# Kernel optimization log

Hardware: AMD Instinct MI355X
Metric: run time of the kernel (lower is better)

Reference implementation:

```python
import jax, jax.numpy as jnp
import numpy as np
import math

N_QUBITS = 8
N_LAYERS = 2
EMBED = 512
HEADS = 64
B, T = 2, 1024


def _ry(state, theta, wire, off):
    # state: (batch?, 2, 2, ..., 2); theta: scalar or (N,)
    ax = off + wire
    st = jnp.moveaxis(state, ax, -1)
    s0, s1 = st[..., 0], st[..., 1]
    half = jnp.asarray(theta) * 0.5
    c, s = jnp.cos(half), jnp.sin(half)
    if c.ndim:  # batched angles -> broadcast over remaining qubit axes
        c = c.reshape((-1,) + (1,) * (s0.ndim - 1))
        s = s.reshape((-1,) + (1,) * (s0.ndim - 1))
    new = jnp.stack([c * s0 - s * s1, s * s0 + c * s1], axis=-1)
    return jnp.moveaxis(new, -1, ax)


def _cnot(state, cw, tw, off):
    st = jnp.moveaxis(state, (off + cw, off + tw), (-2, -1))
    new = jnp.stack([st[..., 0, :], st[..., 1, ::-1]], axis=-2)
    return jnp.moveaxis(new, (-2, -1), (off + cw, off + tw))


def _entangling_state(params):
    # Fixed-parameter block applied to |0...0>: single shared statevector.
    n = N_QUBITS
    psi = jnp.zeros((2,) * n, dtype=params.dtype).at[(0,) * n].set(1.0)
    for l in range(N_LAYERS):
        for q in range(n):
            psi = _ry(psi, params[l, q], q, 0)
        for q in range(n - 1):
            psi = _cnot(psi, q, q + 1, 0)
        psi = _cnot(psi, n - 1, 0, 0)
    return psi


def _quantum_heads(angles, params):
    # angles: (N, n_qubits) data-encoding RY angles; returns (N, n_qubits) <Z_q>.
    n = N_QUBITS
    psi0 = _entangling_state(params)
    state = jnp.broadcast_to(psi0, (angles.shape[0],) + (2,) * n)
    for q in range(n):
        state = _ry(state, angles[:, q], q, 1)
    probs = state * state  # real statevector -> probabilities
    zs = []
    for q in range(n):
        axes = tuple(a for a in range(1, n + 1) if a != q + 1)
        m = probs.sum(axes)  # (N, 2)
        zs.append(m[:, 0] - m[:, 1])
    return jnp.stack(zs, axis=-1)


def setup_inputs() -> dict:
    key = jax.random.key(0)
    kx, kq, kk, kv, kp = jax.random.split(key, 5)
    scale = 1.0 / math.sqrt(EMBED)
    return {
        "x": jax.random.normal(kx, (B, T, EMBED), dtype=jnp.float32),
        "Wq": jax.random.normal(kq, (EMBED, EMBED), dtype=jnp.float32) * scale,
        "Wk": jax.random.normal(kk, (EMBED, EMBED), dtype=jnp.float32) * scale,
        "Wv": jax.random.normal(kv, (EMBED, EMBED), dtype=jnp.float32) * scale,
        "params": jax.random.normal(kp, (N_LAYERS, N_QUBITS), dtype=jnp.float32),
    }


def reference(x, Wq, Wk, Wv, params):
    Bx, Tx, E = x.shape
    head_dim = E // HEADS
    q = x @ Wq.T
    k = x @ Wk.T
    v = x @ Wv.T
    # NOTE: attention on the full embed dim (no head split), scaled by sqrt(E).
    scores = jnp.einsum("bte,bse->bts", q, k) / jnp.sqrt(jnp.asarray(E, x.dtype))
    weights = jax.nn.softmax(scores, axis=-1)
    out = jnp.einsum("bts,bse->bte", weights, v)
    heads = out.reshape(Bx, Tx, HEADS, head_dim)[..., :N_QUBITS]
    angles = heads.reshape(-1, N_QUBITS)  # (B*T*HEADS, n_qubits)
    z = _quantum_heads(angles, params)
    return z.reshape(Bx, Tx, HEADS * N_QUBITS)
```

## Files before the change

kernel.cpp:

```cpp
#include <hip/hip_runtime.h>
#include <math.h>

typedef __attribute__((ext_vector_type(8))) short bf16x8;
typedef __attribute__((ext_vector_type(4))) float f32x4;

#define LD 72

__device__ __forceinline__ ushort f2b(float f) {
    unsigned u = __float_as_uint(f);
    return (ushort)((u + 0x7FFFu + ((u >> 16) & 1u)) >> 16);
}

__global__ __launch_bounds__(256) void cvt_kernel(const float* __restrict__ x,
                                                  const float* __restrict__ wq,
                                                  const float* __restrict__ wk,
                                                  const float* __restrict__ wv,
                                                  ushort* __restrict__ xb,
                                                  ushort* __restrict__ wqb,
                                                  ushort* __restrict__ wkb,
                                                  ushort* __restrict__ wvb) {
    const int z = blockIdx.y;
    const float* src = (z == 0) ? x : (z == 1) ? wq : (z == 2) ? wk : wv;
    ushort* dst = (z == 0) ? xb : (z == 1) ? wqb : (z == 2) ? wkb : wvb;
    const int n = (z == 0) ? (2048 * 512) : (512 * 512);
    const int i = (blockIdx.x * 256 + threadIdx.x) * 8;
    if (i >= n) return;
    float4 v0 = *(const float4*)(src + i);
    float4 v1 = *(const float4*)(src + i + 4);
    ushort t[8] = {f2b(v0.x), f2b(v0.y), f2b(v0.z), f2b(v0.w),
                   f2b(v1.x), f2b(v1.y), f2b(v1.z), f2b(v1.w)};
    *(uint4*)(dst + i) = *(uint4*)t;
}

__global__ __launch_bounds__(256) void qconsts_kernel(const float* __restrict__ params,
                                                      float* __restrict__ ab) {
    __shared__ float st[256];
    __shared__ float red[64];
    const int tid = threadIdx.x;
    st[tid] = (tid == 0) ? 1.0f : 0.0f;
    __syncthreads();
    for (int l = 0; l < 2; ++l) {
        for (int q = 0; q < 8; ++q) {
            float h = 0.5f * params[l * 8 + q];
            float c = cosf(h), s = sinf(h);
            int str = 1 << (7 - q);
            if ((tid & str) == 0) {
                float s0 = st[tid], s1 = st[tid + str];
                st[tid]       = c * s0 - s * s1;
                st[tid + str] = s * s0 + c * s1;
            }
            __syncthreads();
        }
        for (int q = 0; q < 8; ++q) {
            int cw = q, tw = (q + 1) & 7;
            int cs = 1 << (7 - cw), ts = 1 << (7 - tw);
            if ((tid & cs) && !(tid & ts)) {
                float a = st[tid], b = st[tid ^ ts];
                st[tid] = b;
                st[tid ^ ts] = a;
            }
            __syncthreads();
        }
    }
    const float amp = st[tid];
    float v[16];
#pragma unroll
    for (int q = 0; q < 8; ++q) {
        int str = 1 << (7 - q);
        v[q]     = amp * amp * ((tid & str) ? -1.0f : 1.0f);
        v[8 + q] = ((tid & str) == 0) ? 2.0f * amp * st[tid ^ str] : 0.0f;
    }
#pragma unroll
    for (int off = 32; off; off >>= 1)
#pragma unroll
        for (int q = 0; q < 16; ++q) v[q] += __shfl_xor(v[q], off);
    const int lane = tid & 63, wid = tid >> 6;
    if (lane == 0)
#pragma unroll
        for (int q = 0; q < 16; ++q) red[wid * 16 + q] = v[q];
    __syncthreads();
    if (tid < 16) ab[tid] = red[tid] + red[16 + tid] + red[32 + tid] + red[48 + tid];
}

__device__ __forceinline__ void load64(const ushort* __restrict__ p, int ld, int k0,
                                       int tid, uint4 r[2]) {
#pragma unroll
    for (int c = 0; c < 2; ++c) {
        int idx = tid + 256 * c;
        int row = idx >> 3, col = (idx & 7) * 8;
        r[c] = *(const uint4*)(p + (size_t)row * ld + k0 + col);
    }
}
__device__ __forceinline__ void store64(short (*S)[LD], int tid, const uint4 r[2]) {
#pragma unroll
    for (int c = 0; c < 2; ++c) {
        int idx = tid + 256 * c;
        int row = idx >> 3, col = (idx & 7) * 8;
        *(uint4*)&S[row][col] = r[c];
    }
}

__device__ __forceinline__ void mfma64(const short (*As)[LD], const short (*Bs)[LD],
                                       f32x4 acc[2][2], int lane, int wr, int wc) {
    const int r = lane & 15, kb = (lane >> 4) * 8;
#pragma unroll
    for (int c = 0; c < 2; ++c) {
        const int k = c * 32 + kb;
        bf16x8 a0 = *(const bf16x8*)&As[wr * 32 + r][k];
        bf16x8 a1 = *(const bf16x8*)&As[wr * 32 + 16 + r][k];
        bf16x8 b0 = *(const bf16x8*)&Bs[wc * 32 + r][k];
        bf16x8 b1 = *(const bf16x8*)&Bs[wc * 32 + 16 + r][k];
        acc[0][0] = __builtin_amdgcn_mfma_f32_16x16x32_bf16(a0, b0, acc[0][0], 0, 0, 0);
        acc[0][1] = __builtin_amdgcn_mfma_f32_16x16x32_bf16(a0, b1, acc[0][1], 0, 0, 0);
        acc[1][0] = __builtin_amdgcn_mfma_f32_16x16x32_bf16(a1, b0, acc[1][0], 0, 0, 0);
        acc[1][1] = __builtin_amdgcn_mfma_f32_16x16x32_bf16(a1, b1, acc[1][1], 0, 0, 0);
    }
}

__global__ __launch_bounds__(256) void qkv_mfma(const ushort* __restrict__ xb,
                                                const ushort* __restrict__ wqb,
                                                const ushort* __restrict__ wkb,
                                                const ushort* __restrict__ wvb,
                                                ushort* __restrict__ qb,
                                                ushort* __restrict__ kb,
                                                ushort* __restrict__ vT) {
    __shared__ short As[2][64][LD];
    __shared__ short Bs[2][64][LD];
    const int tid = threadIdx.x, lane = tid & 63, w = tid >> 6;
    const int wr = w >> 1, wc = w & 1;
    const int z = blockIdx.z;
    int m0, n0, ldc;
    const ushort *A, *B;
    ushort* C;
    if (z < 2) {
        m0 = blockIdx.x << 6;  n0 = blockIdx.y << 6;
        A = xb;  B = (z == 0) ? wqb : wkb;  C = (z == 0) ? qb : kb;  ldc = 512;
    } else {
        m0 = blockIdx.y << 6;  n0 = blockIdx.x << 6;
        A = wvb;  B = xb;  C = vT;  ldc = 2048;
    }
    const ushort* Ap = A + (size_t)m0 * 512;
    const ushort* Bp = B + (size_t)n0 * 512;
    uint4 ra[2], rb[2];
    load64(Ap, 512, 0, tid, ra);
    load64(Bp, 512, 0, tid, rb);
    store64(As[0], tid, ra);
    store64(Bs[0], tid, rb);
    __syncthreads();
    f32x4 acc[2][2] = {};
    for (int t = 0; t < 8; ++t) {
        if (t < 7) {
            load64(Ap, 512, (t + 1) * 64, tid, ra);
            load64(Bp, 512, (t + 1) * 64, tid, rb);
        }
        mfma64(As[t & 1], Bs[t & 1], acc, lane, wr, wc);
        if (t < 7) {
            store64(As[(t & 1) ^ 1], tid, ra);
            store64(Bs[(t & 1) ^ 1], tid, rb);
        }
        __syncthreads();
    }
    const int rb2 = (lane >> 4) << 2, cc = lane & 15;
#pragma unroll
    for (int fr = 0; fr < 2; ++fr)
#pragma unroll
        for (int fc = 0; fc < 2; ++fc) {
            int row = m0 + wr * 32 + fr * 16 + rb2;
            int col = n0 + wc * 32 + fc * 16 + cc;
#pragma unroll
            for (int r = 0; r < 4; ++r)
                C[(size_t)(row + r) * ldc + col] = f2b(acc[fr][fc][r]);
        }
}

__global__ __launch_bounds__(256) void scores_mfma(const ushort* __restrict__ qb,
                                                   const ushort* __restrict__ kb,
                                                   float* __restrict__ sb) {
    __shared__ short As[2][64][LD];
    __shared__ short Bs[2][64][LD];
    const int tid = threadIdx.x, lane = tid & 63, w = tid >> 6;
    const int wr = w >> 1, wc = w & 1;
    const int m0 = blockIdx.x << 6, n0 = blockIdx.y << 6, z = blockIdx.z;
    const ushort* Ap = qb + (size_t)z * 1024 * 512 + (size_t)m0 * 512;
    const ushort* Bp = kb + (size_t)z * 1024 * 512 + (size_t)n0 * 512;
    float* C = sb + (size_t)z * 1024 * 1024;
    uint4 ra[2], rb[2];
    load64(Ap, 512, 0, tid, ra);
    load64(Bp, 512, 0, tid, rb);
    store64(As[0], tid, ra);
    store64(Bs[0], tid, rb);
    __syncthreads();
    f32x4 acc[2][2] = {};
    for (int t = 0; t < 8; ++t) {
        if (t < 7) {
            load64(Ap, 512, (t + 1) * 64, tid, ra);
            load64(Bp, 512, (t + 1) * 64, tid, rb);
        }
        mfma64(As[t & 1], Bs[t & 1], acc, lane, wr, wc);
        if (t < 7) {
            store64(As[(t & 1) ^ 1], tid, ra);
            store64(Bs[(t & 1) ^ 1], tid, rb);
        }
        __syncthreads();
    }
    const float scale = 0.044194173824159216f;
    const int rb2 = (lane >> 4) << 2, cc = lane & 15;
#pragma unroll
    for (int fr = 0; fr < 2; ++fr)
#pragma unroll
        for (int fc = 0; fc < 2; ++fc) {
            int row = m0 + wr * 32 + fr * 16 + rb2;
            int col = n0 + wc * 32 + fc * 16 + cc;
#pragma unroll
            for (int r = 0; r < 4; ++r)
                C[(size_t)(row + r) * 1024 + col] = acc[fr][fc][r] * scale;
        }
}

__global__ __launch_bounds__(256) void softmax_kernel(const float* __restrict__ S,
                                                      ushort* __restrict__ W) {
    const int row = blockIdx.x, tid = threadIdx.x;
    const float* p = S + (size_t)row * 1024;
    float4 v = ((const float4*)p)[tid];
    float m = fmaxf(fmaxf(v.x, v.y), fmaxf(v.z, v.w));
#pragma unroll
    for (int off = 32; off; off >>= 1) m = fmaxf(m, __shfl_xor(m, off));
    __shared__ float sm[4];
    __shared__ float ss[4];
    const int wid = tid >> 6, lane = tid & 63;
    if (lane == 0) sm[wid] = m;
    __syncthreads();
    m = fmaxf(fmaxf(sm[0], sm[1]), fmaxf(sm[2], sm[3]));
    float e0 = expf(v.x - m), e1 = expf(v.y - m), e2 = expf(v.z - m), e3 = expf(v.w - m);
    float s = e0 + e1 + e2 + e3;
#pragma unroll
    for (int off = 32; off; off >>= 1) s += __shfl_xor(s, off);
    if (lane == 0) ss[wid] = s;
    __syncthreads();
    s = ss[0] + ss[1] + ss[2] + ss[3];
    float r = 1.0f / s;
    ushort4 o = {f2b(e0 * r), f2b(e1 * r), f2b(e2 * r), f2b(e3 * r)};
    ((ushort4*)(W + (size_t)row * 1024))[tid] = o;
}

__global__ __launch_bounds__(256) void pv_mfma(const ushort* __restrict__ wb,
                                               const ushort* __restrict__ vT,
                                               float* __restrict__ out,
                                               const float* __restrict__ ab) {
    __shared__ short As[2][32][LD];
    __shared__ short Bs[2][64][LD];
    const int tid = threadIdx.x, lane = tid & 63, w = tid >> 6;
    const int wr = w >> 1, wc = w & 1;
    const int m0 = blockIdx.x << 5, n0 = blockIdx.y << 6, z = blockIdx.z;
    const ushort* Ap = wb + (size_t)z * 1024 * 1024 + (size_t)m0 * 1024;
    const ushort* Bp = vT + (size_t)n0 * 2048 + z * 1024;
    float* C = out + (size_t)z * 1024 * 512;

    uint4 ra, rbv[2];
    const int arow = tid >> 3, acol = (tid & 7) * 8;
    ra = *(const uint4*)(Ap + (size_t)arow * 1024 + acol);
    load64(Bp, 2048, 0, tid, rbv);
    *(uint4*)&As[0][arow][acol] = ra;
    store64(Bs[0], tid, rbv);
    __syncthreads();
    f32x4 acc[2] = {};
    for (int t = 0; t < 16; ++t) {
        if (t < 15) {
            ra = *(const uint4*)(Ap + (size_t)arow * 1024 + (t + 1) * 64 + acol);
            load64(Bp, 2048, (t + 1) * 64, tid, rbv);
        }
        {
            const short (*Asb)[LD] = As[t & 1];
            const short (*Bsb)[LD] = Bs[t & 1];
            const int r = lane & 15, kb = (lane >> 4) * 8;
#pragma unroll
            for (int c = 0; c < 2; ++c) {
                const int k = c * 32 + kb;
                bf16x8 a0 = *(const bf16x8*)&Asb[wr * 16 + r][k];
                bf16x8 b0 = *(const bf16x8*)&Bsb[wc * 32 + r][k];
                bf16x8 b1 = *(const bf16x8*)&Bsb[wc * 32 + 16 + r][k];
                acc[0] = __builtin_amdgcn_mfma_f32_16x16x32_bf16(a0, b0, acc[0], 0, 0, 0);
                acc[1] = __builtin_amdgcn_mfma_f32_16x16x32_bf16(a0, b1, acc[1], 0, 0, 0);
            }
        }
        if (t < 15) {
            *(uint4*)&As[(t & 1) ^ 1][arow][acol] = ra;
            store64(Bs[(t & 1) ^ 1], tid, rbv);
        }
        __syncthreads();
    }
    const float Aq = ab[lane & 7], Bq = ab[8 + (lane & 7)];
    const int rb2 = (lane >> 4) << 2, cc = lane & 15;
#pragma unroll
    for (int fc = 0; fc < 2; ++fc) {
        int row = m0 + wr * 16 + rb2;
        int col = n0 + wc * 32 + fc * 16 + cc;
#pragma unroll
        for (int r = 0; r < 4; ++r) {
            float sn, cs;
            sincosf(acc[fc][r], &sn, &cs);
            C[(size_t)(row + r) * 512 + col] = cs * Aq - sn * Bq;
        }
    }
}

extern "C" void kernel_launch(void* const* d_in, const int* in_sizes, int n_in,
                              void* d_out, int out_size, void* d_ws, size_t ws_size,
                              hipStream_t stream) {
    const float* x      = (const float*)d_in[0];
    const float* Wq     = (const float*)d_in[1];
    const float* Wk     = (const float*)d_in[2];
    const float* Wv     = (const float*)d_in[3];
    const float* params = (const float*)d_in[4];
    float* out = (float*)d_out;

    char* base = (char*)d_ws;
    float*  ab  = (float*)base;
    ushort* xb  = (ushort*)(base + 256);
    ushort* wqb = xb + 2048 * 512;
    ushort* wkb = wqb + 512 * 512;
    ushort* wvb = wkb + 512 * 512;
    ushort* qb  = wvb + 512 * 512;
    ushort* kb  = qb + 2048 * 512;
    ushort* vT  = kb + 2048 * 512;
    float*  sb  = (float*)(vT + 2048 * 512);
    ushort* wb  = (ushort*)(sb + 2 * 1024 * 1024);

    hipLaunchKernelGGL(cvt_kernel, dim3(512, 4), dim3(256), 0, stream,
                       x, Wq, Wk, Wv, xb, wqb, wkb, wvb);
    hipLaunchKernelGGL(qconsts_kernel, dim3(1), dim3(256), 0, stream, params, ab);
    hipLaunchKernelGGL(qkv_mfma, dim3(32, 8, 3), dim3(256), 0, stream,
                       xb, wqb, wkb, wvb, qb, kb, vT);
    hipLaunchKernelGGL(scores_mfma, dim3(16, 16, 2), dim3(256), 0, stream, qb, kb, sb);
    hipLaunchKernelGGL(softmax_kernel, dim3(2048), dim3(256), 0, stream, sb, wb);
    hipLaunchKernelGGL(pv_mfma, dim3(32, 8, 2), dim3(256), 0, stream, wb, vT, out, ab);
}
```

Before: 106.2 us.

## Stage GEMM tiles with direct global-to-LDS loads and XOR swizzle, enlarge tiles

Replaces the register-staged global→LDS copies in all three MFMA GEMMs with global_load_lds direct transfers into an XOR-swizzled unpadded LDS layout. The QKV GEMM moves to 128x128 tiles with 4x4 MFMA fragments per wave, and the PV GEMM to 64x64 tiles. The bf16 conversion and quantum-constant kernels are merged into one launch. This removes VGPR round-trips and one kernel launch, and increases data reuse. The cost is fewer blocks for occupancy and reliance on async LDS load ordering being correct around barriers.

Result: slower. 111.3 us (+4.8%).

```diff
diff --git a/kernel.cpp b/kernel.cpp
--- a/kernel.cpp
+++ b/kernel.cpp
@@ -3,40 +3,108 @@
 
 typedef __attribute__((ext_vector_type(8))) short bf16x8;
 typedef __attribute__((ext_vector_type(4))) float f32x4;
-
-#define LD 72
 
 __device__ __forceinline__ ushort f2b(float f) {
     unsigned u = __float_as_uint(f);
     return (ushort)((u + 0x7FFFu + ((u >> 16) & 1u)) >> 16);
 }
 
-__global__ __launch_bounds__(256) void cvt_kernel(const float* __restrict__ x,
-                                                  const float* __restrict__ wq,
-                                                  const float* __restrict__ wk,
-                                                  const float* __restrict__ wv,
-                                                  ushort* __restrict__ xb,
-                                                  ushort* __restrict__ wqb,
-                                                  ushort* __restrict__ wkb,
-                                                  ushort* __restrict__ wvb) {
-    const int z = blockIdx.y;
-    const float* src = (z == 0) ? x : (z == 1) ? wq : (z == 2) ? wk : wv;
-    ushort* dst = (z == 0) ? xb : (z == 1) ? wqb : (z == 2) ? wkb : wvb;
-    const int n = (z == 0) ? (2048 * 512) : (512 * 512);
-    const int i = (blockIdx.x * 256 + threadIdx.x) * 8;
-    if (i >= n) return;
-    float4 v0 = *(const float4*)(src + i);
-    float4 v1 = *(const float4*)(src + i + 4);
-    ushort t[8] = {f2b(v0.x), f2b(v0.y), f2b(v0.z), f2b(v0.w),
-                   f2b(v1.x), f2b(v1.y), f2b(v1.z), f2b(v1.w)};
-    *(uint4*)(dst + i) = *(uint4*)t;
-}
-
-__global__ __launch_bounds__(256) void qconsts_kernel(const float* __restrict__ params,
-                                                      float* __restrict__ ab) {
+__device__ __forceinline__ void gl16(const ushort* g, ushort* l) {
+    __builtin_amdgcn_global_load_lds((const __attribute__((address_space(1))) void*)g,
+                                     (__attribute__((address_space(3))) void*)l, 16, 0, 0);
+}
+
+__device__ __forceinline__ void stage128(const ushort* g, int ld, ushort* lds,
+                                         int w, int lane) {
+    const int rsub = lane >> 3;
+    const size_t coff = (size_t)(((lane & 7) ^ (rsub & 7)) * 8);
+#pragma unroll
+    for (int ii = 0; ii < 4; ++ii) {
+        const int i = w * 4 + ii;
+        gl16(g + (size_t)(i * 8 + rsub) * ld + coff, lds + i * 512);
+    }
+}
+__device__ __forceinline__ void stage64(const ushort* g, int ld, ushort* lds,
+                                        int w, int lane) {
+    const int rsub = lane >> 3;
+    const size_t coff = (size_t)(((lane & 7) ^ (rsub & 7)) * 8);
+#pragma unroll
+    for (int ii = 0; ii < 2; ++ii) {
+        const int i = w * 2 + ii;
+        gl16(g + (size_t)(i * 8 + rsub) * ld + coff, lds + i * 512);
+    }
+}
+
+__device__ __forceinline__ bf16x8 frag(const ushort* lds, int row0, int c, int lane) {
+    const int r = row0 + (lane & 15);
+    const int slot = (c * 4 + (lane >> 4)) ^ (r & 7);
+    return *(const bf16x8*)(lds + (size_t)r * 64 + slot * 8);
+}
+
+__device__ __forceinline__ void compute128(const ushort* As, const ushort* Bs,
+                                           f32x4 acc[4][4], int lane, int wr, int wc) {
+#pragma unroll
+    for (int c = 0; c < 2; ++c) {
+        bf16x8 a[4], b[4];
+#pragma unroll
+        for (int f = 0; f < 4; ++f) {
+            a[f] = frag(As, wr * 64 + f * 16, c, lane);
+            b[f] = frag(Bs, wc * 64 + f * 16, c, lane);
+        }
+#pragma unroll
+        for (int i = 0; i < 4; ++i)
+#pragma unroll
+            for (int j = 0; j < 4; ++j)
+                acc[i][j] = __builtin_amdgcn_mfma_f32_16x16x32_bf16(a[i], b[j], acc[i][j], 0, 0, 0);
+    }
+}
+
+__device__ __forceinline__ void compute64(const ushort* As, const ushort* Bs,
+                                          f32x4 acc[2][2], int lane, int wr, int wc) {
+#pragma unroll
+    for (int c = 0; c < 2; ++c) {
+        bf16x8 a[2], b[2];
+#pragma unroll
+        for (int f = 0; f < 2; ++f) {
+            a[f] = frag(As, wr * 32 + f * 16, c, lane);
+            b[f] = frag(Bs, wc * 32 + f * 16, c, lane);
+        }
+#pragma unroll
+        for (int i = 0; i < 2; ++i)
+#pragma unroll
+            for (int j = 0; j < 2; ++j)
+                acc[i][j] = __builtin_amdgcn_mfma_f32_16x16x32_bf16(a[i], b[j], acc[i][j], 0, 0, 0);
+    }
+}
+
+__global__ __launch_bounds__(256) void cvtq_kernel(const float* __restrict__ x,
+                                                   const float* __restrict__ wq,
+                                                   const float* __restrict__ wk,
+                                                   const float* __restrict__ wv,
+                                                   const float* __restrict__ params,
+                                                   ushort* __restrict__ xb,
+                                                   ushort* __restrict__ wqb,
+                                                   ushort* __restrict__ wkb,
+                                                   ushort* __restrict__ wvb,
+                                                   float* __restrict__ ab) {
+    const int tid = threadIdx.x;
+    if (blockIdx.y < 4) {
+        const int z = blockIdx.y;
+        const float* src = (z == 0) ? x : (z == 1) ? wq : (z == 2) ? wk : wv;
+        ushort* dst = (z == 0) ? xb : (z == 1) ? wqb : (z == 2) ? wkb : wvb;
+        const int n = (z == 0) ? (2048 * 512) : (512 * 512);
+        const int i = (blockIdx.x * 256 + tid) * 8;
+        if (i >= n) return;
+        float4 v0 = *(const float4*)(src + i);
+        float4 v1 = *(const float4*)(src + i + 4);
+        ushort t[8] = {f2b(v0.x), f2b(v0.y), f2b(v0.z), f2b(v0.w),
+                       f2b(v1.x), f2b(v1.y), f2b(v1.z), f2b(v1.w)};
+        *(uint4*)(dst + i) = *(uint4*)t;
+        return;
+    }
+    if (blockIdx.x != 0) return;
     __shared__ float st[256];
     __shared__ float red[64];
-    const int tid = threadIdx.x;
     st[tid] = (tid == 0) ? 1.0f : 0.0f;
     __syncthreads();
     for (int l = 0; l < 2; ++l) {
@@ -82,41 +150,6 @@
     if (tid < 16) ab[tid] = red[tid] + red[16 + tid] + red[32 + tid] + red[48 + tid];
 }
 
-__device__ __forceinline__ void load64(const ushort* __restrict__ p, int ld, int k0,
-                                       int tid, uint4 r[2]) {
-#pragma unroll
-    for (int c = 0; c < 2; ++c) {
-        int idx = tid + 256 * c;
-        int row = idx >> 3, col = (idx & 7) * 8;
-        r[c] = *(const uint4*)(p + (size_t)row * ld + k0 + col);
-    }
-}
-__device__ __forceinline__ void store64(short (*S)[LD], int tid, const uint4 r[2]) {
-#pragma unroll
-    for (int c = 0; c < 2; ++c) {
-        int idx = tid + 256 * c;
-        int row = idx >> 3, col = (idx & 7) * 8;
-        *(uint4*)&S[row][col] = r[c];
-    }
-}
-
-__device__ __forceinline__ void mfma64(const short (*As)[LD], const short (*Bs)[LD],
-                                       f32x4 acc[2][2], int lane, int wr, int wc) {
-    const int r = lane & 15, kb = (lane >> 4) * 8;
-#pragma unroll
-    for (int c = 0; c < 2; ++c) {
-        const int k = c * 32 + kb;
-        bf16x8 a0 = *(const bf16x8*)&As[wr * 32 + r][k];
-        bf16x8 a1 = *(const bf16x8*)&As[wr * 32 + 16 + r][k];
-        bf16x8 b0 = *(const bf16x8*)&Bs[wc * 32 + r][k];
-        bf16x8 b1 = *(const bf16x8*)&Bs[wc * 32 + 16 + r][k];
-        acc[0][0] = __builtin_amdgcn_mfma_f32_16x16x32_bf16(a0, b0, acc[0][0], 0, 0, 0);
-        acc[0][1] = __builtin_amdgcn_mfma_f32_16x16x32_bf16(a0, b1, acc[0][1], 0, 0, 0);
-        acc[1][0] = __builtin_amdgcn_mfma_f32_16x16x32_bf16(a1, b0, acc[1][0], 0, 0, 0);
-        acc[1][1] = __builtin_amdgcn_mfma_f32_16x16x32_bf16(a1, b1, acc[1][1], 0, 0, 0);
-    }
-}
-
 __global__ __launch_bounds__(256) void qkv_mfma(const ushort* __restrict__ xb,
                                                 const ushort* __restrict__ wqb,
                                                 const ushort* __restrict__ wkb,
@@ -124,8 +157,8 @@
                                                 ushort* __restrict__ qb,
                                                 ushort* __restrict__ kb,
                                                 ushort* __restrict__ vT) {
-    __shared__ short As[2][64][LD];
-    __shared__ short Bs[2][64][LD];
+    __shared__ ushort As[2][128 * 64];
+    __shared__ ushort Bs[2][128 * 64];
     const int tid = threadIdx.x, lane = tid & 63, w = tid >> 6;
     const int wr = w >> 1, wc = w & 1;
     const int z = blockIdx.z;
@@ -133,40 +166,34 @@
     const ushort *A, *B;
     ushort* C;
     if (z < 2) {
-        m0 = blockIdx.x << 6;  n0 = blockIdx.y << 6;
+        m0 = blockIdx.x << 7;  n0 = blockIdx.y << 7;
         A = xb;  B = (z == 0) ? wqb : wkb;  C = (z == 0) ? qb : kb;  ldc = 512;
     } else {
-        m0 = blockIdx.y << 6;  n0 = blockIdx.x << 6;
+        m0 = blockIdx.y << 7;  n0 = blockIdx.x << 7;
         A = wvb;  B = xb;  C = vT;  ldc = 2048;
     }
     const ushort* Ap = A + (size_t)m0 * 512;
     const ushort* Bp = B + (size_t)n0 * 512;
-    uint4 ra[2], rb[2];
-    load64(Ap, 512, 0, tid, ra);
-    load64(Bp, 512, 0, tid, rb);
-    store64(As[0], tid, ra);
-    store64(Bs[0], tid, rb);
-    __syncthreads();
-    f32x4 acc[2][2] = {};
+    stage128(Ap, 512, As[0], w, lane);
+    stage128(Bp, 512, Bs[0], w, lane);
+    __syncthreads();
+    f32x4 acc[4][4] = {};
     for (int t = 0; t < 8; ++t) {
+        const int cur = t & 1;
         if (t < 7) {
-            load64(Ap, 512, (t + 1) * 64, tid, ra);
-            load64(Bp, 512, (t + 1) * 64, tid, rb);
-        }
-        mfma64(As[t & 1], Bs[t & 1], acc, lane, wr, wc);
-        if (t < 7) {
-            store64(As[(t & 1) ^ 1], tid, ra);
-            store64(Bs[(t & 1) ^ 1], tid, rb);
-        }
+            stage128(Ap + (t + 1) * 64, 512, As[cur ^ 1], w, lane);
+            stage128(Bp + (t + 1) * 64, 512, Bs[cur ^ 1], w, lane);
+        }
+        compute128(As[cur], Bs[cur], acc, lane, wr, wc);
         __syncthreads();
     }
     const int rb2 = (lane >> 4) << 2, cc = lane & 15;
 #pragma unroll
-    for (int fr = 0; fr < 2; ++fr)
-#pragma unroll
-        for (int fc = 0; fc < 2; ++fc) {
-            int row = m0 + wr * 32 + fr * 16 + rb2;
-            int col = n0 + wc * 32 + fc * 16 + cc;
+    for (int fr = 0; fr < 4; ++fr)
+#pragma unroll
+        for (int fc = 0; fc < 4; ++fc) {
+            int row = m0 + wr * 64 + fr * 16 + rb2;
+            int col = n0 + wc * 64 + fc * 16 + cc;
 #pragma unroll
             for (int r = 0; r < 4; ++r)
                 C[(size_t)(row + r) * ldc + col] = f2b(acc[fr][fc][r]);
@@ -176,31 +203,25 @@
 __global__ __launch_bounds__(256) void scores_mfma(const ushort* __restrict__ qb,
                                                    const ushort* __restrict__ kb,
                                                    float* __restrict__ sb) {
-    __shared__ short As[2][64][LD];
-    __shared__ short Bs[2][64][LD];
+    __shared__ ushort As[2][64 * 64];
+    __shared__ ushort Bs[2][64 * 64];
     const int tid = threadIdx.x, lane = tid & 63, w = tid >> 6;
     const int wr = w >> 1, wc = w & 1;
     const int m0 = blockIdx.x << 6, n0 = blockIdx.y << 6, z = blockIdx.z;
     const ushort* Ap = qb + (size_t)z * 1024 * 512 + (size_t)m0 * 512;
     const ushort* Bp = kb + (size_t)z * 1024 * 512 + (size_t)n0 * 512;
     float* C = sb + (size_t)z * 1024 * 1024;
-    uint4 ra[2], rb[2];
-    load64(Ap, 512, 0, tid, ra);
-    load64(Bp, 512, 0, tid, rb);
-    store64(As[0], tid, ra);
-    store64(Bs[0], tid, rb);
+    stage64(Ap, 512, As[0], w, lane);
+    stage64(Bp, 512, Bs[0], w, lane);
     __syncthreads();
     f32x4 acc[2][2] = {};
     for (int t = 0; t < 8; ++t) {
+        const int cur = t & 1;
         if (t < 7) {
-            load64(Ap, 512, (t + 1) * 64, tid, ra);
-            load64(Bp, 512, (t + 1) * 64, tid, rb);
-        }
-        mfma64(As[t & 1], Bs[t & 1], acc, lane, wr, wc);
-        if (t < 7) {
-            store64(As[(t & 1) ^ 1], tid, ra);
-            store64(Bs[(t & 1) ^ 1], tid, rb);
-        }
+            stage64(Ap + (t + 1) * 64, 512, As[cur ^ 1], w, lane);
+            stage64(Bp + (t + 1) * 64, 512, Bs[cur ^ 1], w, lane);
+        }
+        compute64(As[cur], Bs[cur], acc, lane, wr, wc);
         __syncthreads();
     }
     const float scale = 0.044194173824159216f;
@@ -247,61 +268,42 @@
                                                const ushort* __restrict__ vT,
                                                float* __restrict__ out,
                                                const float* __restrict__ ab) {
-    __shared__ short As[2][32][LD];
-    __shared__ short Bs[2][64][LD];
+    __shared__ ushort As[2][64 * 64];
+    __shared__ ushort Bs[2][64 * 64];
     const int tid = threadIdx.x, lane = tid & 63, w = tid >> 6;
     const int wr = w >> 1, wc = w & 1;
-    const int m0 = blockIdx.x << 5, n0 = blockIdx.y << 6, z = blockIdx.z;
+    const int m0 = blockIdx.x << 6, n0 = blockIdx.y << 6, z = blockIdx.z;
     const ushort* Ap = wb + (size_t)z * 1024 * 1024 + (size_t)m0 * 1024;
     const ushort* Bp = vT + (size_t)n0 * 2048 + z * 1024;
     float* C = out + (size_t)z * 1024 * 512;
-
-    uint4 ra, rbv[2];
-    const int arow = tid >> 3, acol = (tid & 7) * 8;
-    ra = *(const uint4*)(Ap + (size_t)arow * 1024 + acol);
-    load64(Bp, 2048, 0, tid, rbv);
-    *(uint4*)&As[0][arow][acol] = ra;
-    store64(Bs[0], tid, rbv);
-    __syncthreads();
-    f32x4 acc[2] = {};
+    stage64(Ap, 1024, As[0], w, lane);
+    stage64(Bp, 2048, Bs[0], w, lane);
+    __syncthreads();
+    f32x4 acc[2][2] = {};
     for (int t = 0; t < 16; ++t) {
+        const int cur = t & 1;
         if (t < 15) {
-            ra = *(const uint4*)(Ap + (size_t)arow * 1024 + (t + 1) * 64 + acol);
-            load64(Bp, 2048, (t + 1) * 64, tid, rbv);
-        }
-        {
-            const short (*Asb)[LD] = As[t & 1];
-            const short (*Bsb)[LD] = Bs[t & 1];
-            const int r = lane & 15, kb = (lane >> 4) * 8;
-#pragma unroll
-            for (int c = 0; c < 2; ++c) {
-                const int k = c * 32 + kb;
-                bf16x8 a0 = *(const bf16x8*)&Asb[wr * 16 + r][k];
-                bf16x8 b0 = *(const bf16x8*)&Bsb[wc * 32 + r][k];
-                bf16x8 b1 = *(const bf16x8*)&Bsb[wc * 32 + 16 + r][k];
-                acc[0] = __builtin_amdgcn_mfma_f32_16x16x32_bf16(a0, b0, acc[0], 0, 0, 0);
-                acc[1] = __builtin_amdgcn_mfma_f32_16x16x32_bf16(a0, b1, acc[1], 0, 0, 0);
-            }
-        }
-        if (t < 15) {
-            *(uint4*)&As[(t & 1) ^ 1][arow][acol] = ra;
-            store64(Bs[(t & 1) ^ 1], tid, rbv);
-        }
+            stage64(Ap + (t + 1) * 64, 1024, As[cur ^ 1], w, lane);
+            stage64(Bp + (t + 1) * 64, 2048, Bs[cur ^ 1], w, lane);
+        }
+        compute64(As[cur], Bs[cur], acc, lane, wr, wc);
         __syncthreads();
     }
     const float Aq = ab[lane & 7], Bq = ab[8 + (lane & 7)];
     const int rb2 = (lane >> 4) << 2, cc = lane & 15;
 #pragma unroll
-    for (int fc = 0; fc < 2; ++fc) {
-        int row = m0 + wr * 16 + rb2;
-        int col = n0 + wc * 32 + fc * 16 + cc;
-#pragma unroll
-        for (int r = 0; r < 4; ++r) {
-            float sn, cs;
-            sincosf(acc[fc][r], &sn, &cs);
-            C[(size_t)(row + r) * 512 + col] = cs * Aq - sn * Bq;
-        }
-    }
+    for (int fr = 0; fr < 2; ++fr)
+#pragma unroll
+        for (int fc = 0; fc < 2; ++fc) {
+            int row = m0 + wr * 32 + fr * 16 + rb2;
+            int col = n0 + wc * 32 + fc * 16 + cc;
+#pragma unroll
+            for (int r = 0; r < 4; ++r) {
+                float sn, cs;
+                sincosf(acc[fr][fc][r], &sn, &cs);
+                C[(size_t)(row + r) * 512 + col] = cs * Aq - sn * Bq;
+            }
+        }
 }
 
 extern "C" void kernel_launch(void* const* d_in, const int* in_sizes, int n_in,
@@ -326,12 +328,11 @@
     float*  sb  = (float*)(vT + 2048 * 512);
     ushort* wb  = (ushort*)(sb + 2 * 1024 * 1024);
 
-    hipLaunchKernelGGL(cvt_kernel, dim3(512, 4), dim3(256), 0, stream,
-                       x, Wq, Wk, Wv, xb, wqb, wkb, wvb);
-    hipLaunchKernelGGL(qconsts_kernel, dim3(1), dim3(256), 0, stream, params, ab);
-    hipLaunchKernelGGL(qkv_mfma, dim3(32, 8, 3), dim3(256), 0, stream,
+    hipLaunchKernelGGL(cvtq_kernel, dim3(512, 5), dim3(256), 0, stream,
+                       x, Wq, Wk, Wv, params, xb, wqb, wkb, wvb, ab);
+    hipLaunchKernelGGL(qkv_mfma, dim3(16, 4, 3), dim3(256), 0, stream,
                        xb, wqb, wkb, wvb, qb, kb, vT);
     hipLaunchKernelGGL(scores_mfma, dim3(16, 16, 2), dim3(256), 0, stream, qb, kb, sb);
     hipLaunchKernelGGL(softmax_kernel, dim3(2048), dim3(256), 0, stream, sb, wb);
-    hipLaunchKernelGGL(pv_mfma, dim3(32, 8, 2), dim3(256), 0, stream, wb, vT, out, ab);
-}
+    hipLaunchKernelGGL(pv_mfma, dim3(16, 8, 2), dim3(256), 0, stream, wb, vT, out, ab);
+}
```
